# Optimization experiments

Hardware: AMD Instinct MI355X
Metric: run time of the kernel (lower is better)

## Reference

```python
import jax, jax.numpy as jnp
import numpy as np

NC_MEM = 64          # nTemporalMemoryChannels
NC_IMG = 64          # nImageFeatureChannels
FTL_RATIO = 0.5      # temporalFTLRatio
N_BLOCKS = 3         # nTemporalBlocks
B, H, W = 32, 64, 96
M = 32               # memory buffer length (= max(memory_idx)+1)


def setup_inputs() -> dict:
    key = jax.random.key(0)
    ks = jax.random.split(key, 8)
    eye = jnp.eye(4, dtype=jnp.float32)
    img_features = jax.random.normal(ks[0], (B, NC_IMG, H, W), jnp.float32)
    prev_mem_features = jax.random.normal(ks[1], (M, NC_MEM, H, W), jnp.float32)
    # extrinsics: random perturbation around identity so torch.inverse-equivalent is well conditioned
    prev_extrinsics = 0.1 * jax.random.normal(ks[2], (M, 4, 4), jnp.float32) + eye
    cur_extrinsics = 0.1 * jax.random.normal(ks[3], (B, 4, 4), jnp.float32) + eye
    memory_idx = jnp.arange(B, dtype=jnp.int32)
    use_memory = jax.random.randint(ks[4], (B,), 0, 2).astype(bool)
    NC = NC_MEM + NC_IMG
    Ws = jax.random.normal(ks[5], (N_BLOCKS, NC, NC), jnp.float32) * (1.0 / np.sqrt(NC))
    bs = jax.random.normal(ks[6], (N_BLOCKS, NC), jnp.float32) * 0.01
    return {
        "img_features": img_features,
        "prev_mem_features": prev_mem_features,
        "prev_extrinsics": prev_extrinsics,
        "cur_extrinsics": cur_extrinsics,
        "memory_idx": memory_idx,
        "use_memory": use_memory,
        "Ws": Ws,
        "bs": bs,
    }


def _apply_ftl(xf, feats, ratio):
    # Feature Transform Layer: first `ratio` fraction of channels (rounded down
    # to a multiple of 4) treated as groups of homogeneous 4-vectors per pixel,
    # warped by the 4x4 transform xf; remaining channels pass through.
    b, c, h, w = feats.shape
    nc_ftl = (int(c * ratio) // 4) * 4
    g = nc_ftl // 4
    pts = feats[:, :nc_ftl].reshape(b, g, 4, h * w)
    pts = jnp.einsum("bij,bgjp->bgip", xf, pts).reshape(b, nc_ftl, h, w)
    return jnp.concatenate([pts, feats[:, nc_ftl:]], axis=1)


def reference(img_features, prev_mem_features, prev_extrinsics, cur_extrinsics,
              memory_idx, use_memory, Ws, bs):
    eye = jnp.eye(4, dtype=prev_extrinsics.dtype)
    # --- transform_memory_features (gather + extrinsics warp, masked) ---
    mem_g = prev_mem_features[memory_idx]              # [B, NC_MEM, H, W]
    prev_ext_g = prev_extrinsics[memory_idx]           # [B, 4, 4]
    # entries with use_memory=False are zeroed; guard inverse with identity
    safe_prev = jnp.where(use_memory[:, None, None], prev_ext_g, eye)
    prev_cam0_to_world = jnp.linalg.inv(safe_prev)
    xf = jnp.einsum("bij,bjk->bik", cur_extrinsics, prev_cam0_to_world)
    mem_xfed = _apply_ftl(xf, mem_g, FTL_RATIO)
    mem_xfed = jnp.where(use_memory[:, None, None, None], mem_xfed,
                         jnp.zeros((), mem_xfed.dtype))
    # --- forward_one_step: concat + 1x1 conv stack (pointwise matmuls) ---
    x = jnp.concatenate([mem_xfed, img_features], axis=1)  # [B, 128, H, W]
    n = Ws.shape[0]
    for i in range(n):
        x = jnp.einsum("oc,bchw->bohw", Ws[i], x) + bs[i][None, :, None, None]
        if i != n - 1:
            x = jax.nn.relu(x)
    fused_features = x[:, NC_MEM:]                     # returned output
    return fused_features
```

## Files before the change

### kernel.cpp

```cpp
#include <hip/hip_runtime.h>

#define NC_MEM 64
#define NC_IMG 64
#define NC     128
#define B_     32
#define H_     64
#define W_     96
#define HW_    (H_ * W_)
#define P_TILE 64
#define NTILES (HW_ / P_TILE)
#define RS     136

#define WA_HI  0
#define WA_LO  98304
#define XF_OFF 196608
#define UM_OFF 198656

typedef __attribute__((ext_vector_type(8))) short bf16x8;
typedef __attribute__((ext_vector_type(4))) float f32x4;

__device__ inline unsigned short f2bf_rn(float x) {
    unsigned u = __float_as_uint(x);
    return (unsigned short)((u + 0x7FFFu + ((u >> 16) & 1u)) >> 16);
}
__device__ inline float bf2f(unsigned short h) {
    return __uint_as_float(((unsigned)h) << 16);
}

__global__ void prep(const float* __restrict__ Ws,
                     const float* __restrict__ prev_ext,
                     const float* __restrict__ cur_ext,
                     const int* __restrict__ mem_idx,
                     const unsigned char* __restrict__ um_raw,
                     unsigned char* __restrict__ wsb) {
    if (blockIdx.x < 192) {
        int idx = blockIdx.x * 256 + threadIdx.x;
        int l = idx >> 14, r = idx & 16383, o = r >> 7, c = r & 127;
        float w = Ws[idx];
        unsigned short hi = f2bf_rn(w);
        unsigned short lo = f2bf_rn(w - bf2f(hi));
        int mt = o >> 4, lm = o & 15, ks = c >> 5, kr = c & 31, q = kr >> 3, j = kr & 7;
        int lane = q * 16 + lm;
        int di = ((((l * 8 + mt) * 4 + ks) * 64 + lane) << 3) + j;
        ((unsigned short*)(wsb + WA_HI))[di] = hi;
        ((unsigned short*)(wsb + WA_LO))[di] = lo;
        return;
    }
    int b = threadIdx.x;
    if (b >= B_) return;

    bool is_bool = false;
    for (int i = 0; i < 32; ++i)
        if ((i & 3) && um_raw[i]) is_bool = true;
    bool um = is_bool ? (um_raw[b] != 0) : (((const int*)um_raw)[b] != 0);
    int mi = mem_idx[b];

    float a[16];
#pragma unroll
    for (int i = 0; i < 16; ++i)
        a[i] = um ? prev_ext[mi * 16 + i] : ((i % 5 == 0) ? 1.f : 0.f);

    float s0 = a[0]*a[5]  - a[1]*a[4];
    float s1 = a[0]*a[6]  - a[2]*a[4];
    float s2 = a[0]*a[7]  - a[3]*a[4];
    float s3 = a[1]*a[6]  - a[2]*a[5];
    float s4 = a[1]*a[7]  - a[3]*a[5];
    float s5 = a[2]*a[7]  - a[3]*a[6];
    float c5 = a[10]*a[15] - a[11]*a[14];
    float c4 = a[9]*a[15]  - a[11]*a[13];
    float c3 = a[9]*a[14]  - a[10]*a[13];
    float c2 = a[8]*a[15]  - a[11]*a[12];
    float c1 = a[8]*a[14]  - a[10]*a[12];
    float c0 = a[8]*a[13]  - a[9]*a[12];
    float det = s0*c5 - s1*c4 + s2*c3 + s3*c2 - s4*c1 + s5*c0;
    float id = 1.0f / det;

    float inv[16];
    inv[0]  = ( a[5]*c5  - a[6]*c4  + a[7]*c3)  * id;
    inv[1]  = (-a[1]*c5  + a[2]*c4  - a[3]*c3)  * id;
    inv[2]  = ( a[13]*s5 - a[14]*s4 + a[15]*s3) * id;
    inv[3]  = (-a[9]*s5  + a[10]*s4 - a[11]*s3) * id;
    inv[4]  = (-a[4]*c5  + a[6]*c2  - a[7]*c1)  * id;
    inv[5]  = ( a[0]*c5  - a[2]*c2  + a[3]*c1)  * id;
    inv[6]  = (-a[12]*s5 + a[14]*s2 - a[15]*s1) * id;
    inv[7]  = ( a[8]*s5  - a[10]*s2 + a[11]*s1) * id;
    inv[8]  = ( a[4]*c4  - a[5]*c2  + a[7]*c0)  * id;
    inv[9]  = (-a[0]*c4  + a[1]*c2  - a[3]*c0)  * id;
    inv[10] = ( a[12]*s4 - a[13]*s2 + a[15]*s0) * id;
    inv[11] = (-a[8]*s4  + a[9]*s2  - a[11]*s0) * id;
    inv[12] = (-a[4]*c3  + a[5]*c1  - a[6]*c0)  * id;
    inv[13] = ( a[0]*c3  - a[1]*c1  + a[2]*c0)  * id;
    inv[14] = (-a[12]*s3 + a[13]*s1 - a[14]*s0) * id;
    inv[15] = ( a[8]*s3  - a[9]*s1  + a[10]*s0) * id;

    float* xf = (float*)(wsb + XF_OFF) + b * 16;
#pragma unroll
    for (int i = 0; i < 4; ++i)
#pragma unroll
        for (int j2 = 0; j2 < 4; ++j2) {
            float s = 0.f;
#pragma unroll
            for (int k = 0; k < 4; ++k)
                s += cur_ext[b * 16 + i * 4 + k] * inv[k * 4 + j2];
            xf[i * 4 + j2] = s;
        }
    ((float*)(wsb + UM_OFF))[b] = um ? 1.f : 0.f;
}

__global__ __launch_bounds__(256, 4)
void fused_main(const float* __restrict__ img, const float* __restrict__ mem,
                const int* __restrict__ mem_idx, const float* __restrict__ bs,
                const unsigned char* __restrict__ wsb, float* __restrict__ out) {
    __shared__ unsigned short xh[64 * RS];
    __shared__ unsigned short xl[64 * RS];

    const int t   = threadIdx.x;
    const int b   = blockIdx.y;
    const int hw0 = blockIdx.x * P_TILE;
    const bool umb = ((const float*)(wsb + UM_OFF))[b] != 0.f;
    const int mi  = mem_idx[b];

    const bf16x8* __restrict__ WH = (const bf16x8*)(wsb + WA_HI);
    const bf16x8* __restrict__ WL = (const bf16x8*)(wsb + WA_LO);

    {
        const int px = t & 63, cq = t >> 6;
        float xfv[16];
        if (umb) {
            const float* xfp = (const float*)(wsb + XF_OFF) + b * 16;
#pragma unroll
            for (int i = 0; i < 16; ++i) xfv[i] = xfp[i];
        }
        const int pstart = umb ? 0 : 4;
        for (int p = pstart; p < 8; ++p) {
            int gg = p * 4 + cq;
            int c0 = gg * 4;
            const float* src = (c0 < 64)
                ? (mem + ((size_t)mi * 64 + c0) * HW_ + hw0 + px)
                : (img + ((size_t)b  * 64 + (c0 - 64)) * HW_ + hw0 + px);
            float v0 = src[0], v1 = src[HW_], v2 = src[2 * HW_], v3 = src[3 * HW_];
            if (umb && gg < 8) {
                float r0 = xfv[0]  * v0 + xfv[1]  * v1 + xfv[2]  * v2 + xfv[3]  * v3;
                float r1 = xfv[4]  * v0 + xfv[5]  * v1 + xfv[6]  * v2 + xfv[7]  * v3;
                float r2 = xfv[8]  * v0 + xfv[9]  * v1 + xfv[10] * v2 + xfv[11] * v3;
                float r3 = xfv[12] * v0 + xfv[13] * v1 + xfv[14] * v2 + xfv[15] * v3;
                v0 = r0; v1 = r1; v2 = r2; v3 = r3;
            }
            unsigned u0 = __float_as_uint(v0), u1 = __float_as_uint(v1);
            unsigned u2 = __float_as_uint(v2), u3 = __float_as_uint(v3);
            unsigned l0 = __float_as_uint(v0 - __uint_as_float(u0 & 0xFFFF0000u));
            unsigned l1 = __float_as_uint(v1 - __uint_as_float(u1 & 0xFFFF0000u));
            unsigned l2 = __float_as_uint(v2 - __uint_as_float(u2 & 0xFFFF0000u));
            unsigned l3 = __float_as_uint(v3 - __uint_as_float(u3 & 0xFFFF0000u));
            uint2 hp = make_uint2(__builtin_amdgcn_perm(u1, u0, 0x07060302u),
                                  __builtin_amdgcn_perm(u3, u2, 0x07060302u));
            uint2 lp = make_uint2(__builtin_amdgcn_perm(l1, l0, 0x07060302u),
                                  __builtin_amdgcn_perm(l3, l2, 0x07060302u));
            *(uint2*)&xh[px * RS + c0] = hp;
            *(uint2*)&xl[px * RS + c0] = lp;
        }
    }
    __syncthreads();

    const int w    = t >> 6;
    const int lane = t & 63;
    const int q    = lane >> 4;
    const int lm   = lane & 15;

    const int mt0 = 2 * w;
#pragma unroll
    for (int l = 0; l < 2; ++l) {
        f32x4 acc[2][4];
#pragma unroll
        for (int mi2 = 0; mi2 < 2; ++mi2) {
            f32x4 bv = *(const f32x4*)&bs[l * NC + (mt0 + mi2) * 16 + q * 4];
#pragma unroll
            for (int nt = 0; nt < 4; ++nt) acc[mi2][nt] = bv;
        }
        auto do_ks = [&](int ks) {
            int f0 = ((l * 8 + mt0) * 4 + ks) * 64 + lane;
            int f1 = ((l * 8 + mt0 + 1) * 4 + ks) * 64 + lane;
            bf16x8 ah0 = WH[f0], al0 = WL[f0];
            bf16x8 ah1 = WH[f1], al1 = WL[f1];
#pragma unroll
            for (int nt = 0; nt < 4; ++nt) {
                bf16x8 bh = *(const bf16x8*)&xh[(nt * 16 + lm) * RS + ks * 32 + q * 8];
                bf16x8 bl = *(const bf16x8*)&xl[(nt * 16 + lm) * RS + ks * 32 + q * 8];
                acc[0][nt] = __builtin_amdgcn_mfma_f32_16x16x32_bf16(ah0, bh, acc[0][nt], 0, 0, 0);
                acc[1][nt] = __builtin_amdgcn_mfma_f32_16x16x32_bf16(ah1, bh, acc[1][nt], 0, 0, 0);
                acc[0][nt] = __builtin_amdgcn_mfma_f32_16x16x32_bf16(al0, bh, acc[0][nt], 0, 0, 0);
                acc[1][nt] = __builtin_amdgcn_mfma_f32_16x16x32_bf16(al1, bh, acc[1][nt], 0, 0, 0);
                acc[0][nt] = __builtin_amdgcn_mfma_f32_16x16x32_bf16(ah0, bl, acc[0][nt], 0, 0, 0);
                acc[1][nt] = __builtin_amdgcn_mfma_f32_16x16x32_bf16(ah1, bl, acc[1][nt], 0, 0, 0);
            }
        };
        if (l == 0 && !umb) { do_ks(2); do_ks(3); }
        else { do_ks(0); do_ks(1); do_ks(2); do_ks(3); }

        __syncthreads();
#pragma unroll
        for (int mi2 = 0; mi2 < 2; ++mi2) {
            int o0 = (mt0 + mi2) * 16 + q * 4;
#pragma unroll
            for (int nt = 0; nt < 4; ++nt) {
                int ppx = nt * 16 + lm;
                float v0 = fmaxf(acc[mi2][nt][0], 0.f);
                float v1 = fmaxf(acc[mi2][nt][1], 0.f);
                float v2 = fmaxf(acc[mi2][nt][2], 0.f);
                float v3 = fmaxf(acc[mi2][nt][3], 0.f);
                unsigned u0 = __float_as_uint(v0), u1 = __float_as_uint(v1);
                unsigned u2 = __float_as_uint(v2), u3 = __float_as_uint(v3);
                unsigned l0 = __float_as_uint(v0 - __uint_as_float(u0 & 0xFFFF0000u));
                unsigned l1 = __float_as_uint(v1 - __uint_as_float(u1 & 0xFFFF0000u));
                unsigned l2 = __float_as_uint(v2 - __uint_as_float(u2 & 0xFFFF0000u));
                unsigned l3 = __float_as_uint(v3 - __uint_as_float(u3 & 0xFFFF0000u));
                *(uint2*)&xh[ppx * RS + o0] =
                    make_uint2(__builtin_amdgcn_perm(u1, u0, 0x07060302u),
                               __builtin_amdgcn_perm(u3, u2, 0x07060302u));
                *(uint2*)&xl[ppx * RS + o0] =
                    make_uint2(__builtin_amdgcn_perm(l1, l0, 0x07060302u),
                               __builtin_amdgcn_perm(l3, l2, 0x07060302u));
            }
        }
        __syncthreads();
    }

    {
        const int mt2 = 4 + w;
        f32x4 acc[4];
        f32x4 bv = *(const f32x4*)&bs[2 * NC + mt2 * 16 + q * 4];
#pragma unroll
        for (int nt = 0; nt < 4; ++nt) acc[nt] = bv;
#pragma unroll
        for (int ks = 0; ks < 4; ++ks) {
            int f = ((2 * 8 + mt2) * 4 + ks) * 64 + lane;
            bf16x8 ah = WH[f], al = WL[f];
#pragma unroll
            for (int nt = 0; nt < 4; ++nt) {
                bf16x8 bh = *(const bf16x8*)&xh[(nt * 16 + lm) * RS + ks * 32 + q * 8];
                bf16x8 bl = *(const bf16x8*)&xl[(nt * 16 + lm) * RS + ks * 32 + q * 8];
                acc[nt] = __builtin_amdgcn_mfma_f32_16x16x32_bf16(ah, bh, acc[nt], 0, 0, 0);
                acc[nt] = __builtin_amdgcn_mfma_f32_16x16x32_bf16(al, bh, acc[nt], 0, 0, 0);
                acc[nt] = __builtin_amdgcn_mfma_f32_16x16x32_bf16(ah, bl, acc[nt], 0, 0, 0);
            }
        }
        const int oc0 = mt2 * 16 + q * 4 - 64;
#pragma unroll
        for (int nt = 0; nt < 4; ++nt) {
            float* dst = out + ((size_t)b * 64 + oc0) * HW_ + hw0 + nt * 16 + lm;
#pragma unroll
            for (int r = 0; r < 4; ++r)
                dst[(size_t)r * HW_] = acc[nt][r];
        }
    }
}

extern "C" void kernel_launch(void* const* d_in, const int* in_sizes, int n_in,
                              void* d_out, int out_size, void* d_ws, size_t ws_size,
                              hipStream_t stream) {
    const float* img  = (const float*)d_in[0];
    const float* mem  = (const float*)d_in[1];
    const float* pext = (const float*)d_in[2];
    const float* cext = (const float*)d_in[3];
    const int*   midx = (const int*)d_in[4];
    const unsigned char* umem = (const unsigned char*)d_in[5];
    const float* Ws   = (const float*)d_in[6];
    const float* bs   = (const float*)d_in[7];
    float* out = (float*)d_out;
    unsigned char* wsb = (unsigned char*)d_ws;

    hipLaunchKernelGGL(prep, dim3(193), dim3(256), 0, stream,
                       Ws, pext, cext, midx, umem, wsb);
    hipLaunchKernelGGL(fused_main, dim3(NTILES, B_), dim3(256), 0, stream,
                       img, mem, midx, bs, wsb, out);
}
```

Measured before the change: 175.9 us.

## Double pixel tile to 128 with 512 threads and MFMA-fragment-native LDS layout

The pixel tile per block grows from 64 to 128 and the block from 256 to 512 threads. Each group of four waves handles half the pixels, so every weight fragment loaded from global memory feeds twice as many pixels. The shared-memory activation buffer is relaid out so each 16-pixel by 32-channel MFMA B-fragment is one contiguous chunk read with lane*8 addressing, with padding to avoid bank conflicts. LDS per block roughly doubles, which may reduce how many blocks fit on a CU, and the grid is halved.

```diff
diff --git a/kernel.cpp b/kernel.cpp
--- a/kernel.cpp
+++ b/kernel.cpp
@@ -7,9 +7,10 @@
 #define H_     64
 #define W_     96
 #define HW_    (H_ * W_)
-#define P_TILE 64
+#define P_TILE 128
 #define NTILES (HW_ / P_TILE)
-#define RS     136
+#define FS     520
+#define FOFF(pt, ks) ((((pt) * 4) + (ks)) * FS)
 
 #define WA_HI  0
 #define WA_LO  98304
@@ -107,12 +108,12 @@
     ((float*)(wsb + UM_OFF))[b] = um ? 1.f : 0.f;
 }
 
-__global__ __launch_bounds__(256, 4)
+__global__ __launch_bounds__(512, 4)
 void fused_main(const float* __restrict__ img, const float* __restrict__ mem,
                 const int* __restrict__ mem_idx, const float* __restrict__ bs,
                 const unsigned char* __restrict__ wsb, float* __restrict__ out) {
-    __shared__ unsigned short xh[64 * RS];
-    __shared__ unsigned short xl[64 * RS];
+    __shared__ unsigned short xh[32 * FS];
+    __shared__ unsigned short xl[32 * FS];
 
     const int t   = threadIdx.x;
     const int b   = blockIdx.y;
@@ -123,8 +124,12 @@
     const bf16x8* __restrict__ WH = (const bf16x8*)(wsb + WA_HI);
     const bf16x8* __restrict__ WL = (const bf16x8*)(wsb + WA_LO);
 
+    const int w    = t >> 6;
+    const int lane = t & 63;
+
     {
-        const int px = t & 63, cq = t >> 6;
+        const int px = lane + 64 * (w & 1);
+        const int cq = t >> 7;
         float xfv[16];
         if (umb) {
             const float* xfp = (const float*)(wsb + XF_OFF) + b * 16;
@@ -156,36 +161,37 @@
                                   __builtin_amdgcn_perm(u3, u2, 0x07060302u));
             uint2 lp = make_uint2(__builtin_amdgcn_perm(l1, l0, 0x07060302u),
                                   __builtin_amdgcn_perm(l3, l2, 0x07060302u));
-            *(uint2*)&xh[px * RS + c0] = hp;
-            *(uint2*)&xl[px * RS + c0] = lp;
+            int addr = FOFF(px >> 4, c0 >> 5) + (((c0 & 31) >> 3) * 16 + (px & 15)) * 8 + (c0 & 7);
+            *(uint2*)&xh[addr] = hp;
+            *(uint2*)&xl[addr] = lp;
         }
     }
     __syncthreads();
 
-    const int w    = t >> 6;
-    const int lane = t & 63;
-    const int q    = lane >> 4;
-    const int lm   = lane & 15;
-
-    const int mt0 = 2 * w;
+    const int wq = lane >> 4;
+    const int lm = lane & 15;
+
+    const int mt0 = 2 * (w & 3);
+    const int nt0 = 4 * (w >> 2);
 #pragma unroll
     for (int l = 0; l < 2; ++l) {
         f32x4 acc[2][4];
 #pragma unroll
         for (int mi2 = 0; mi2 < 2; ++mi2) {
-            f32x4 bv = *(const f32x4*)&bs[l * NC + (mt0 + mi2) * 16 + q * 4];
+            f32x4 bv = *(const f32x4*)&bs[l * NC + (mt0 + mi2) * 16 + wq * 4];
 #pragma unroll
             for (int nt = 0; nt < 4; ++nt) acc[mi2][nt] = bv;
         }
         auto do_ks = [&](int ks) {
             int f0 = ((l * 8 + mt0) * 4 + ks) * 64 + lane;
-            int f1 = ((l * 8 + mt0 + 1) * 4 + ks) * 64 + lane;
+            int f1 = f0 + 4 * 64;
             bf16x8 ah0 = WH[f0], al0 = WL[f0];
             bf16x8 ah1 = WH[f1], al1 = WL[f1];
 #pragma unroll
             for (int nt = 0; nt < 4; ++nt) {
-                bf16x8 bh = *(const bf16x8*)&xh[(nt * 16 + lm) * RS + ks * 32 + q * 8];
-                bf16x8 bl = *(const bf16x8*)&xl[(nt * 16 + lm) * RS + ks * 32 + q * 8];
+                int ba = FOFF(nt0 + nt, ks) + lane * 8;
+                bf16x8 bh = *(const bf16x8*)&xh[ba];
+                bf16x8 bl = *(const bf16x8*)&xl[ba];
                 acc[0][nt] = __builtin_amdgcn_mfma_f32_16x16x32_bf16(ah0, bh, acc[0][nt], 0, 0, 0);
                 acc[1][nt] = __builtin_amdgcn_mfma_f32_16x16x32_bf16(ah1, bh, acc[1][nt], 0, 0, 0);
                 acc[0][nt] = __builtin_amdgcn_mfma_f32_16x16x32_bf16(al0, bh, acc[0][nt], 0, 0, 0);
@@ -200,10 +206,12 @@
         __syncthreads();
 #pragma unroll
         for (int mi2 = 0; mi2 < 2; ++mi2) {
-            int o0 = (mt0 + mi2) * 16 + q * 4;
+            int mt = mt0 + mi2;
+            int ks2 = mt >> 1;
+            int lane_f = ((mt & 1) * 2 + (wq >> 1)) * 16 + lm;
+            int j0 = (wq & 1) * 4;
 #pragma unroll
             for (int nt = 0; nt < 4; ++nt) {
-                int ppx = nt * 16 + lm;
                 float v0 = fmaxf(acc[mi2][nt][0], 0.f);
                 float v1 = fmaxf(acc[mi2][nt][1], 0.f);
                 float v2 = fmaxf(acc[mi2][nt][2], 0.f);
@@ -214,10 +222,11 @@
                 unsigned l1 = __float_as_uint(v1 - __uint_as_float(u1 & 0xFFFF0000u));
                 unsigned l2 = __float_as_uint(v2 - __uint_as_float(u2 & 0xFFFF0000u));
                 unsigned l3 = __float_as_uint(v3 - __uint_as_float(u3 & 0xFFFF0000u));
-                *(uint2*)&xh[ppx * RS + o0] =
+                int addr = FOFF(nt0 + nt, ks2) + lane_f * 8 + j0;
+                *(uint2*)&xh[addr] =
                     make_uint2(__builtin_amdgcn_perm(u1, u0, 0x07060302u),
                                __builtin_amdgcn_perm(u3, u2, 0x07060302u));
-                *(uint2*)&xl[ppx * RS + o0] =
+                *(uint2*)&xl[addr] =
                     make_uint2(__builtin_amdgcn_perm(l1, l0, 0x07060302u),
                                __builtin_amdgcn_perm(l3, l2, 0x07060302u));
             }
@@ -226,9 +235,9 @@
     }
 
     {
-        const int mt2 = 4 + w;
+        const int mt2 = 4 + (w & 3);
         f32x4 acc[4];
-        f32x4 bv = *(const f32x4*)&bs[2 * NC + mt2 * 16 + q * 4];
+        f32x4 bv = *(const f32x4*)&bs[2 * NC + mt2 * 16 + wq * 4];
 #pragma unroll
         for (int nt = 0; nt < 4; ++nt) acc[nt] = bv;
 #pragma unroll
@@ -237,17 +246,18 @@
             bf16x8 ah = WH[f], al = WL[f];
 #pragma unroll
             for (int nt = 0; nt < 4; ++nt) {
-                bf16x8 bh = *(const bf16x8*)&xh[(nt * 16 + lm) * RS + ks * 32 + q * 8];
-                bf16x8 bl = *(const bf16x8*)&xl[(nt * 16 + lm) * RS + ks * 32 + q * 8];
+                int ba = FOFF(nt0 + nt, ks) + lane * 8;
+                bf16x8 bh = *(const bf16x8*)&xh[ba];
+                bf16x8 bl = *(const bf16x8*)&xl[ba];
                 acc[nt] = __builtin_amdgcn_mfma_f32_16x16x32_bf16(ah, bh, acc[nt], 0, 0, 0);
                 acc[nt] = __builtin_amdgcn_mfma_f32_16x16x32_bf16(al, bh, acc[nt], 0, 0, 0);
                 acc[nt] = __builtin_amdgcn_mfma_f32_16x16x32_bf16(ah, bl, acc[nt], 0, 0, 0);
             }
         }
-        const int oc0 = mt2 * 16 + q * 4 - 64;
+        const int oc0 = mt2 * 16 + wq * 4 - 64;
 #pragma unroll
         for (int nt = 0; nt < 4; ++nt) {
-            float* dst = out + ((size_t)b * 64 + oc0) * HW_ + hw0 + nt * 16 + lm;
+            float* dst = out + ((size_t)b * 64 + oc0) * HW_ + hw0 + (nt0 + nt) * 16 + lm;
 #pragma unroll
             for (int r = 0; r < 4; ++r)
                 dst[(size_t)r * HW_] = acc[nt][r];
@@ -271,6 +281,6 @@
 
     hipLaunchKernelGGL(prep, dim3(193), dim3(256), 0, stream,
                        Ws, pext, cext, midx, umem, wsb);
-    hipLaunchKernelGGL(fused_main, dim3(NTILES, B_), dim3(256), 0, stream,
+    hipLaunchKernelGGL(fused_main, dim3(NTILES, B_), dim3(512), 0, stream,
                        img, mem, midx, bs, wsb, out);
 }
```

After: 176.8 us. About the same (+0.6%).
